# Kernel tuning notes

Hardware: AMD Instinct MI355X
Metric: run time of the kernel (lower is better)

The kernel has to match this reference:

```python
import jax, jax.numpy as jnp
import numpy as np

N = 100000   # nodes
E = 1600000  # edges
F = 128      # in_feats
H = 4        # heads
D = 32       # out_feats per head
NEG_SLOPE = 0.2


def setup_inputs() -> dict:
    key = jax.random.key(0)
    k1, k2, k3, k4, k5, k6 = jax.random.split(key, 6)
    feat = jax.random.normal(k1, (N, F), dtype=jnp.float32)
    W = jax.random.normal(k2, (H * D, F), dtype=jnp.float32) * (1.0 / np.sqrt(F))
    attn_l = jax.random.normal(k3, (1, H, D), dtype=jnp.float32) * 0.1
    attn_r = jax.random.normal(k4, (1, H, D), dtype=jnp.float32) * 0.1
    src = jax.random.randint(k5, (E,), 0, N, dtype=jnp.int32)
    dst = jax.random.randint(k6, (E,), 0, N, dtype=jnp.int32)
    return {"feat": feat, "W": W, "attn_l": attn_l, "attn_r": attn_r, "src": src, "dst": dst}


def reference(feat, W, attn_l, attn_r, src, dst):
    # fc projection: [N, F] -> [N, H, D]
    h = (feat @ W.T).reshape(N, H, D)
    # per-node attention logits [N, H]
    el = jnp.sum(h * attn_l, axis=-1)
    er = jnp.sum(h * attn_r, axis=-1)
    # edge scores: el[src] + er[dst] -> leaky relu  [E, H]
    e = jax.nn.leaky_relu(el[src] + er[dst], negative_slope=NEG_SLOPE)
    # segment softmax over edges grouped by destination node, per head
    m = jax.ops.segment_max(e, dst, num_segments=N)          # [N, H]
    ex = jnp.exp(e - m[dst])                                 # [E, H]
    s = jax.ops.segment_sum(ex, dst, num_segments=N)         # [N, H]
    alpha = ex / s[dst]                                      # [E, H]
    # weighted sparse aggregation: out[dst] += alpha * h[src]
    msgs = alpha[:, :, None] * h[src]                        # [E, H, D]
    rst = jax.ops.segment_sum(msgs, dst, num_segments=N)     # [N, H, D]
    return rst
```

## Files before the change

### kernel.cpp

```cpp
#include <hip/hip_runtime.h>

constexpr int N_NODES = 100000;
constexpr int E_EDGES = 1600000;
constexpr int NBLK    = (N_NODES + 1023) / 1024;

typedef _Float16 f16;
typedef _Float16 f16x2 __attribute__((ext_vector_type(2)));
typedef _Float16 f16x4 __attribute__((ext_vector_type(4)));
typedef _Float16 f16x8 __attribute__((ext_vector_type(8)));
typedef float f32x4 __attribute__((ext_vector_type(4)));

__global__ __launch_bounds__(256) void k_gemm(const float* __restrict__ feat,
                                              const float* __restrict__ W,
                                              const float* __restrict__ attn_l,
                                              const float* __restrict__ attn_r,
                                              f16* __restrict__ h2,
                                              float* __restrict__ el,
                                              float* __restrict__ er) {
    __shared__ f16 Wlds[128 * 128];
    char* wb = (char*)Wlds;
    const int tid = threadIdx.x;

    {
        int n = tid >> 1;
        int kh = (tid & 1) * 64;
        const float* wsrc = W + n * 128 + kh;
#pragma unroll
        for (int q = 0; q < 8; ++q) {
            float4 u0 = *reinterpret_cast<const float4*>(wsrc + q * 8);
            float4 u1 = *reinterpret_cast<const float4*>(wsrc + q * 8 + 4);
            f16x8 v;
            v[0] = (f16)u0.x; v[1] = (f16)u0.y; v[2] = (f16)u0.z; v[3] = (f16)u0.w;
            v[4] = (f16)u1.x; v[5] = (f16)u1.y; v[6] = (f16)u1.z; v[7] = (f16)u1.w;
            unsigned byte = (unsigned)(n * 256 + kh * 2 + q * 16) ^ ((n & 7) << 4);
            *reinterpret_cast<f16x8*>(wb + byte) = v;
        }
    }
    __syncthreads();

    const int wav  = tid >> 6;
    const int lane = tid & 63;
    const int la = lane & 15;
    const int lb = lane >> 4;
    const int row0w = blockIdx.x * 64 + wav * 16;

    f16x8 ffrag[4];
    {
        int rowA = row0w + la;
        if (rowA >= N_NODES) rowA = N_NODES - 1;
        const float* ap = feat + (size_t)rowA * 128 + lb * 8;
#pragma unroll
        for (int kk = 0; kk < 4; ++kk) {
            float4 u0 = *reinterpret_cast<const float4*>(ap + kk * 32);
            float4 u1 = *reinterpret_cast<const float4*>(ap + kk * 32 + 4);
            f16x8 a;
            a[0] = (f16)u0.x; a[1] = (f16)u0.y; a[2] = (f16)u0.z; a[3] = (f16)u0.w;
            a[4] = (f16)u1.x; a[5] = (f16)u1.y; a[6] = (f16)u1.z; a[7] = (f16)u1.w;
            ffrag[kk] = a;
        }
    }

    f32x4 acc[8];
#pragma unroll
    for (int t = 0; t < 8; ++t) acc[t] = (f32x4){0.f, 0.f, 0.f, 0.f};

#pragma unroll
    for (int t = 0; t < 8; ++t) {
        int wrow = t * 16 + la;
#pragma unroll
        for (int kk = 0; kk < 4; ++kk) {
            unsigned byte = (unsigned)(wrow * 256 + (kk * 32 + lb * 8) * 2) ^ ((wrow & 7) << 4);
            f16x8 b = *reinterpret_cast<const f16x8*>(wb + byte);
            acc[t] = __builtin_amdgcn_mfma_f32_16x16x32_f16(b, ffrag[kk], acc[t], 0, 0, 0);
        }
    }

    const int row = row0w + la;
    const bool ok = row < N_NODES;
    if (ok) {
#pragma unroll
        for (int t = 0; t < 8; ++t) {
            f16x4 hv;
            hv.x = (f16)acc[t][0]; hv.y = (f16)acc[t][1];
            hv.z = (f16)acc[t][2]; hv.w = (f16)acc[t][3];
            *reinterpret_cast<f16x4*>(&h2[(size_t)row * 128 + t * 16 + lb * 4]) = hv;
        }
    }

    float sl[4] = {0.f, 0.f, 0.f, 0.f}, sr[4] = {0.f, 0.f, 0.f, 0.f};
#pragma unroll
    for (int t = 0; t < 8; ++t) {
        float4 alv = reinterpret_cast<const float4*>(attn_l)[t * 4 + lb];
        float4 arv = reinterpret_cast<const float4*>(attn_r)[t * 4 + lb];
        int g = t >> 1;
        sl[g] += acc[t][0] * alv.x + acc[t][1] * alv.y + acc[t][2] * alv.z + acc[t][3] * alv.w;
        sr[g] += acc[t][0] * arv.x + acc[t][1] * arv.y + acc[t][2] * arv.z + acc[t][3] * arv.w;
    }
#pragma unroll
    for (int g = 0; g < 4; ++g) {
        sl[g] += __shfl_xor(sl[g], 16, 64);
        sl[g] += __shfl_xor(sl[g], 32, 64);
        sr[g] += __shfl_xor(sr[g], 16, 64);
        sr[g] += __shfl_xor(sr[g], 32, 64);
    }
    if (lb == 0 && ok) {
        *reinterpret_cast<float4*>(el + (size_t)row * 4) = make_float4(sl[0], sl[1], sl[2], sl[3]);
        *reinterpret_cast<float4*>(er + (size_t)row * 4) = make_float4(sr[0], sr[1], sr[2], sr[3]);
    }
}

__global__ void k_hist(const int4* __restrict__ dst4, int* __restrict__ deg,
                       int4* __restrict__ rank4) {
    int t = blockIdx.x * blockDim.x + threadIdx.x;
    if (t < E_EDGES / 4) {
        int4 d = dst4[t];
        int r0 = atomicAdd(&deg[d.x], 1);
        int r1 = atomicAdd(&deg[d.y], 1);
        int r2 = atomicAdd(&deg[d.z], 1);
        int r3 = atomicAdd(&deg[d.w], 1);
        rank4[t] = make_int4(r0, r1, r2, r3);
    }
}

__global__ void k_bsum(const int* __restrict__ deg, int* __restrict__ aux) {
    int tid = threadIdx.x;
    int i0 = blockIdx.x * 1024 + tid * 4;
    int sum = 0;
#pragma unroll
    for (int j = 0; j < 4; ++j)
        if (i0 + j < N_NODES) sum += (deg[i0 + j] + 3) & ~3;
#pragma unroll
    for (int m = 32; m; m >>= 1) sum += __shfl_xor(sum, m, 64);
    __shared__ int wsums[4];
    if ((tid & 63) == 0) wsums[tid >> 6] = sum;
    __syncthreads();
    if (tid == 0) aux[blockIdx.x] = wsums[0] + wsums[1] + wsums[2] + wsums[3];
}

__global__ void k_scanaux(int* __restrict__ aux) {
    __shared__ int s[128];
    int i = threadIdx.x;
    int v = (i < NBLK) ? aux[i] : 0;
    s[i] = v;
    __syncthreads();
#pragma unroll
    for (int d = 1; d < 128; d <<= 1) {
        int t = (i >= d) ? s[i - d] : 0;
        __syncthreads();
        s[i] += t;
        __syncthreads();
    }
    if (i < NBLK) aux[i] = s[i] - v;
}

__global__ void k_bscan(const int* __restrict__ deg, const int* __restrict__ aux,
                        int* __restrict__ start, int* __restrict__ ssrc,
                        f16* __restrict__ h2, float* __restrict__ el) {
    if (blockIdx.x == 0 && threadIdx.x == 0) {
        float4 z = make_float4(0.f, 0.f, 0.f, 0.f);
        float4* hrow = reinterpret_cast<float4*>(h2 + (size_t)N_NODES * 128);
#pragma unroll
        for (int q = 0; q < 16; ++q) hrow[q] = z;
        *reinterpret_cast<float4*>(el + (size_t)N_NODES * 4) =
            make_float4(-1e4f, -1e4f, -1e4f, -1e4f);
    }
    int tid = threadIdx.x;
    int lane = tid & 63;
    int wid = tid >> 6;
    int i0 = blockIdx.x * 1024 + tid * 4;
    int v[4], pv[4];
#pragma unroll
    for (int j = 0; j < 4; ++j) {
        v[j]  = (i0 + j < N_NODES) ? deg[i0 + j] : 0;
        pv[j] = (v[j] + 3) & ~3;
    }
    int tsum = pv[0] + pv[1] + pv[2] + pv[3];
    int x = tsum;
#pragma unroll
    for (int d = 1; d < 64; d <<= 1) {
        int t = __shfl_up(x, d, 64);
        if (lane >= d) x += t;
    }
    __shared__ int wsums[4];
    if (lane == 63) wsums[wid] = x;
    __syncthreads();
    int base = aux[blockIdx.x];
#pragma unroll
    for (int w = 0; w < 4; ++w)
        if (w < wid) base += wsums[w];
    int p = base + x - tsum;
#pragma unroll
    for (int j = 0; j < 4; ++j) {
        if (i0 + j < N_NODES) {
            start[i0 + j] = p;
            for (int q = v[j]; q < pv[j]; ++q) ssrc[p + q] = N_NODES;
        }
        p += pv[j];
    }
}

__global__ void k_scatter(const int4* __restrict__ src4, const int4* __restrict__ dst4,
                          const int4* __restrict__ rank4, const int* __restrict__ start,
                          int* __restrict__ ssrc) {
    int t = blockIdx.x * blockDim.x + threadIdx.x;
    if (t >= E_EDGES / 4) return;
    int4 s = src4[t];
    int4 d = dst4[t];
    int4 r = rank4[t];
    int p0 = start[d.x] + r.x;
    int p1 = start[d.y] + r.y;
    int p2 = start[d.z] + r.z;
    int p3 = start[d.w] + r.w;
    ssrc[p0] = s.x;
    ssrc[p1] = s.y;
    ssrc[p2] = s.z;
    ssrc[p3] = s.w;
}

__global__ __launch_bounds__(128) void k_aggr(const f16* __restrict__ h2,
                                              const float* __restrict__ el,
                                              const float* __restrict__ er,
                                              const int* __restrict__ ssrc,
                                              const int* __restrict__ start,
                                              const int* __restrict__ deg,
                                              float* __restrict__ out) {
    int n = blockIdx.x * 2 + (threadIdx.x >> 6);
    if (n >= N_NODES) return;
    int lane = threadIdx.x & 63;
    int half = lane >> 5;
    int l5 = lane & 31;
    int g = l5 >> 3;
    int d = deg[n];
    int nit = ((d + 3) & ~3) >> 2;
    int s4 = __builtin_amdgcn_readfirstlane(start[n] >> 2);
    const int4* ssrc4 = reinterpret_cast<const int4*>(ssrc);
    float ern = er[n * 4 + g];

    f16x4 acA = {0, 0, 0, 0}, acB = {0, 0, 0, 0};
    float swA = 0.f, swB = 0.f;

    if (nit > 0) {
        int4 sv = ssrc4[s4];
        for (int it = 0; it < nit; ++it) {
            int4 svn = ssrc4[s4 + it + 1];

            int nA = half ? sv.y : sv.x;
            int nB = half ? sv.w : sv.z;
            float eA = el[(size_t)nA * 4 + g];
            float eB = el[(size_t)nB * 4 + g];
            f16x4 qA = *reinterpret_cast<const f16x4*>(h2 + (size_t)nA * 128 + l5 * 4);
            f16x4 qB = *reinterpret_cast<const f16x4*>(h2 + (size_t)nB * 128 + l5 * 4);

            float xA = eA + ern; xA = fmaxf(xA, 0.2f * xA);
            float xB = eB + ern; xB = fmaxf(xB, 0.2f * xB);
            float wA = __expf(xA);
            float wB = __expf(xB);

            f16 hA = (f16)wA; f16x4 wvA = {hA, hA, hA, hA};
            f16 hB = (f16)wB; f16x4 wvB = {hB, hB, hB, hB};
            acA += wvA * qA; swA += wA;
            acB += wvB * qB; swB += wB;

            sv = svn;
        }
    }

    f16x4 ac = acA + acB;
    float swv = swA + swB;
    union { f16x4 v; int u[2]; } uu; uu.v = ac;
    int o0 = __shfl_xor(uu.u[0], 32, 64);
    int o1 = __shfl_xor(uu.u[1], 32, 64);
    union { int u[2]; f16x4 v; } vv; vv.u[0] = o0; vv.u[1] = o1;
    ac += vv.v;
    swv += __shfl_xor(swv, 32, 64);

    float inv = (d > 0) ? 1.0f / swv : 0.0f;
    if (half == 0) {
        float4 o = make_float4((float)ac[0] * inv, (float)ac[1] * inv,
                               (float)ac[2] * inv, (float)ac[3] * inv);
        *reinterpret_cast<float4*>(out + (size_t)n * 128 + l5 * 4) = o;
    }
}

extern "C" void kernel_launch(void* const* d_in, const int* in_sizes, int n_in,
                              void* d_out, int out_size, void* d_ws, size_t ws_size,
                              hipStream_t stream) {
    const float* feat   = (const float*)d_in[0];
    const float* W      = (const float*)d_in[1];
    const float* attn_l = (const float*)d_in[2];
    const float* attn_r = (const float*)d_in[3];
    const int*   src    = (const int*)d_in[4];
    const int*   dst    = (const int*)d_in[5];
    float* out = (float*)d_out;

    f16*   h2    = (f16*)d_ws;
    float* el    = (float*)(h2 + (size_t)(N_NODES + 8) * 128);
    float* er    = el + (size_t)(N_NODES + 4) * 4;
    int*   deg   = (int*)(er + (size_t)N_NODES * 4);
    int*   start = deg + N_NODES;
    int*   rank  = start + N_NODES;
    int*   ssrc  = rank + E_EDGES;
    int*   aux   = ssrc + E_EDGES + 3 * N_NODES + 64;

    hipMemsetAsync(deg, 0, N_NODES * sizeof(int), stream);

    k_hist<<<(E_EDGES / 4 + 255) / 256, 256, 0, stream>>>((const int4*)dst, deg, (int4*)rank);
    k_gemm<<<(N_NODES + 63) / 64, 256, 0, stream>>>(feat, W, attn_l, attn_r, h2, el, er);
    k_bsum<<<NBLK, 256, 0, stream>>>(deg, aux);
    k_scanaux<<<1, 128, 0, stream>>>(aux);
    k_bscan<<<NBLK, 256, 0, stream>>>(deg, aux, start, ssrc, h2, el);
    k_scatter<<<(E_EDGES / 4 + 255) / 256, 256, 0, stream>>>(
        (const int4*)src, (const int4*)dst, (const int4*)rank, start, ssrc);
    k_aggr<<<(N_NODES + 1) / 2, 128, 0, stream>>>(h2, el, er, ssrc, start, deg, out);
}
```

Before: 213.5 us.

## Fuse histogram into GEMM kernel and fold aux scan into block scan

Merges the degree histogram and the projection GEMM into one launch. Odd and even blocks run the two phases in opposite order so that atomic-bound work and compute-bound work overlap. Removes the single-block aux scan kernel: each k_bscan block instead reduces the aux prefix for itself with one wavefront. This cuts two launches and their serialization, at the cost of a larger fused kernel whose LDS footprint may limit how many blocks the histogram phase gets.

```diff
diff --git a/kernel.cpp b/kernel.cpp
--- a/kernel.cpp
+++ b/kernel.cpp
@@ -3,6 +3,7 @@
 constexpr int N_NODES = 100000;
 constexpr int E_EDGES = 1600000;
 constexpr int NBLK    = (N_NODES + 1023) / 1024;
+constexpr int NBLOCKS = (N_NODES + 63) / 64;
 
 typedef _Float16 f16;
 typedef _Float16 f16x2 __attribute__((ext_vector_type(2)));
@@ -10,17 +11,30 @@
 typedef _Float16 f16x8 __attribute__((ext_vector_type(8)));
 typedef float f32x4 __attribute__((ext_vector_type(4)));
 
-__global__ __launch_bounds__(256) void k_gemm(const float* __restrict__ feat,
-                                              const float* __restrict__ W,
-                                              const float* __restrict__ attn_l,
-                                              const float* __restrict__ attn_r,
-                                              f16* __restrict__ h2,
-                                              float* __restrict__ el,
-                                              float* __restrict__ er) {
-    __shared__ f16 Wlds[128 * 128];
+__device__ __forceinline__ void hist_phase(int bid, int tid,
+                                           const int4* __restrict__ dst4,
+                                           int* __restrict__ deg,
+                                           int4* __restrict__ rank4) {
+    int t = bid * 256 + tid;
+    if (t < E_EDGES / 4) {
+        int4 d = dst4[t];
+        int r0 = atomicAdd(&deg[d.x], 1);
+        int r1 = atomicAdd(&deg[d.y], 1);
+        int r2 = atomicAdd(&deg[d.z], 1);
+        int r3 = atomicAdd(&deg[d.w], 1);
+        rank4[t] = make_int4(r0, r1, r2, r3);
+    }
+}
+
+__device__ __forceinline__ void gemm_phase(int bid, int tid, f16* Wlds,
+                                           const float* __restrict__ feat,
+                                           const float* __restrict__ W,
+                                           const float* __restrict__ attn_l,
+                                           const float* __restrict__ attn_r,
+                                           f16* __restrict__ h2,
+                                           float* __restrict__ el,
+                                           float* __restrict__ er) {
     char* wb = (char*)Wlds;
-    const int tid = threadIdx.x;
-
     {
         int n = tid >> 1;
         int kh = (tid & 1) * 64;
@@ -42,7 +56,7 @@
     const int lane = tid & 63;
     const int la = lane & 15;
     const int lb = lane >> 4;
-    const int row0w = blockIdx.x * 64 + wav * 16;
+    const int row0w = bid * 64 + wav * 16;
 
     f16x8 ffrag[4];
     {
@@ -109,16 +123,21 @@
     }
 }
 
-__global__ void k_hist(const int4* __restrict__ dst4, int* __restrict__ deg,
-                       int4* __restrict__ rank4) {
-    int t = blockIdx.x * blockDim.x + threadIdx.x;
-    if (t < E_EDGES / 4) {
-        int4 d = dst4[t];
-        int r0 = atomicAdd(&deg[d.x], 1);
-        int r1 = atomicAdd(&deg[d.y], 1);
-        int r2 = atomicAdd(&deg[d.z], 1);
-        int r3 = atomicAdd(&deg[d.w], 1);
-        rank4[t] = make_int4(r0, r1, r2, r3);
+__global__ __launch_bounds__(256) void k_gemm_hist(
+        const float* __restrict__ feat, const float* __restrict__ W,
+        const float* __restrict__ attn_l, const float* __restrict__ attn_r,
+        f16* __restrict__ h2, float* __restrict__ el, float* __restrict__ er,
+        const int4* __restrict__ dst4, int* __restrict__ deg,
+        int4* __restrict__ rank4) {
+    __shared__ f16 Wlds[128 * 128];
+    const int bid = blockIdx.x;
+    const int tid = threadIdx.x;
+    if (bid & 1) {
+        hist_phase(bid, tid, dst4, deg, rank4);
+        gemm_phase(bid, tid, Wlds, feat, W, attn_l, attn_r, h2, el, er);
+    } else {
+        gemm_phase(bid, tid, Wlds, feat, W, attn_l, attn_r, h2, el, er);
+        hist_phase(bid, tid, dst4, deg, rank4);
     }
 }
 
@@ -135,22 +154,6 @@
     if ((tid & 63) == 0) wsums[tid >> 6] = sum;
     __syncthreads();
     if (tid == 0) aux[blockIdx.x] = wsums[0] + wsums[1] + wsums[2] + wsums[3];
-}
-
-__global__ void k_scanaux(int* __restrict__ aux) {
-    __shared__ int s[128];
-    int i = threadIdx.x;
-    int v = (i < NBLK) ? aux[i] : 0;
-    s[i] = v;
-    __syncthreads();
-#pragma unroll
-    for (int d = 1; d < 128; d <<= 1) {
-        int t = (i >= d) ? s[i - d] : 0;
-        __syncthreads();
-        s[i] += t;
-        __syncthreads();
-    }
-    if (i < NBLK) aux[i] = s[i] - v;
 }
 
 __global__ void k_bscan(const int* __restrict__ deg, const int* __restrict__ aux,
@@ -167,6 +170,17 @@
     int tid = threadIdx.x;
     int lane = tid & 63;
     int wid = tid >> 6;
+
+    __shared__ int sbase;
+    if (tid < 64) {
+        int a = 0;
+        if (tid < blockIdx.x) a += aux[tid];
+        if (tid + 64 < blockIdx.x) a += aux[tid + 64];
+#pragma unroll
+        for (int m = 32; m; m >>= 1) a += __shfl_xor(a, m, 64);
+        if (tid == 0) sbase = a;
+    }
+
     int i0 = blockIdx.x * 1024 + tid * 4;
     int v[4], pv[4];
 #pragma unroll
@@ -184,7 +198,7 @@
     __shared__ int wsums[4];
     if (lane == 63) wsums[wid] = x;
     __syncthreads();
-    int base = aux[blockIdx.x];
+    int base = sbase;
 #pragma unroll
     for (int w = 0; w < 4; ++w)
         if (w < wid) base += wsums[w];
@@ -304,10 +318,9 @@
 
     hipMemsetAsync(deg, 0, N_NODES * sizeof(int), stream);
 
-    k_hist<<<(E_EDGES / 4 + 255) / 256, 256, 0, stream>>>((const int4*)dst, deg, (int4*)rank);
-    k_gemm<<<(N_NODES + 63) / 64, 256, 0, stream>>>(feat, W, attn_l, attn_r, h2, el, er);
+    k_gemm_hist<<<NBLOCKS, 256, 0, stream>>>(feat, W, attn_l, attn_r, h2, el, er,
+                                             (const int4*)dst, deg, (int4*)rank);
     k_bsum<<<NBLK, 256, 0, stream>>>(deg, aux);
-    k_scanaux<<<1, 128, 0, stream>>>(aux);
     k_bscan<<<NBLK, 256, 0, stream>>>(deg, aux, start, ssrc, h2, el);
     k_scatter<<<(E_EDGES / 4 + 255) / 256, 256, 0, stream>>>(
         (const int4*)src, (const int4*)dst, (const int4*)rank, start, ssrc);
```

Result: faster. 188.4 us, median of 2 (-11.8%).
